# Performance work log

Hardware: AMD Instinct MI355X
Metric: run time of the kernel (lower is better)

Reference implementation:

```python
import jax, jax.numpy as jnp
import numpy as np

K = 8       # out_caps
H = 64      # nhidden
TAU = 1.0

def _l2norm(x, eps=1e-12):
    n = jnp.linalg.norm(x, axis=-1, keepdims=True)
    return x / jnp.maximum(n, eps)

def setup_inputs() -> dict:
    key = jax.random.key(0)
    k1, k2, k3, k4 = jax.random.split(key, 4)
    B, N, NB, D = 128, 50, 32, K * H
    return {
        "self_vectors": jax.random.normal(k1, (B, N, D), dtype=jnp.float32),
        "neighbor_vectors": jax.random.normal(k2, (B, N, NB, D), dtype=jnp.float32),
        "W1": jax.random.normal(k3, (D, D), dtype=jnp.float32) * 0.04,
        "b1": jax.random.normal(k4, (D,), dtype=jnp.float32) * 0.01,
        "max_iter": 3,
    }

def reference(self_vectors, neighbor_vectors, W1, b1, max_iter):
    B, N, _ = self_vectors.shape
    NB = neighbor_vectors.shape[2]
    # fc1 + ReLU projections (dropout p=0 -> identity)
    self_z = jax.nn.relu(self_vectors @ W1.T + b1)            # [B,N,K*H]
    neigh_z = jax.nn.relu(neighbor_vectors @ W1.T + b1)       # [B,N,NB,K*H]
    s = _l2norm(self_z.reshape(B, N, K, H))                   # [B,N,K,H]
    nz = _l2norm(neigh_z.reshape(B, N, NB, K, H))             # [B,N,NB,K,H]
    u = None
    for it in range(max_iter):
        if u is None:
            p = jnp.zeros((B, N, NB, K), dtype=s.dtype)
        else:
            p = jnp.einsum('bnmkh,bnkh->bnmk', nz, u)
        p = jax.nn.softmax(p / TAU, axis=-1)                   # softmax over K
        u = jnp.einsum('bnmkh,bnmk->bnkh', nz, p) + s          # sum over neighbors
        if it < max_iter - 1:
            u = _l2norm(u)
    return jax.nn.relu(u.reshape(B, N, K * H))
```

## Files before the change

### kernel.cpp

```cpp
#include <hip/hip_runtime.h>
#include <hip/hip_bf16.h>


#define D_DIM 512
#define BM 64
#define BK 32
#define KSTEPS 16

typedef __attribute__((ext_vector_type(8))) short short8;
typedef __attribute__((ext_vector_type(4))) short short4v;
typedef __attribute__((ext_vector_type(4))) float f32x4;

static __device__ __forceinline__ short f2bf(float f) {
    __bf16 b = (__bf16)f;
    return __builtin_bit_cast(short, b);
}
static __device__ __forceinline__ float bf2f(short s) {
    unsigned u = ((unsigned)(unsigned short)s) << 16;
    return __builtin_bit_cast(float, u);
}
static __device__ __forceinline__ void gload_lds16(const void* g, void* l) {
    __builtin_amdgcn_global_load_lds(
        (const __attribute__((address_space(1))) void*)g,
        (__attribute__((address_space(3))) void*)l, 16, 0, 0);
}

__global__ __launch_bounds__(256) void wconv(const float* __restrict__ W,
                                             short* __restrict__ Wb) {
    const int i = (blockIdx.x * 256 + threadIdx.x) * 8;
    const float4 v0 = *reinterpret_cast<const float4*>(W + i);
    const float4 v1 = *reinterpret_cast<const float4*>(W + i + 4);
    short8 o;
    o[0] = f2bf(v0.x); o[1] = f2bf(v0.y); o[2] = f2bf(v0.z); o[3] = f2bf(v0.w);
    o[4] = f2bf(v1.x); o[5] = f2bf(v1.y); o[6] = f2bf(v1.z); o[7] = f2bf(v1.w);
    *reinterpret_cast<short8*>(Wb + i) = o;
}

template <bool FUSED>
__global__ __launch_bounds__(256, 2) void gemm_route(
    const float* __restrict__ A,
    const short* __restrict__ Wb,
    const float* __restrict__ bias,
    short* __restrict__ Zs,
    const short* __restrict__ S,
    const int* __restrict__ miter_ptr,
    float* __restrict__ out)
{
    __shared__ __align__(16) char smem[81920];
    float* const lAf32 = (float*)smem;
    short* const lB = (short*)(smem + 16384);

    const int t = threadIdx.x;
    const int lane = t & 63;
    const int wid = t >> 6;
    const size_t row0 = (size_t)blockIdx.x * BM;
    const int wc = wid * 128;
    const int l15 = lane & 15;

    const int cb = wc + l15;
    float bcol[8];
    #pragma unroll
    for (int n = 0; n < 8; ++n) bcol[n] = bias[cb + n * 16];
    int miter = 0;
    if (FUSED) miter = *miter_ptr;

    auto stage = [&](int step, int buf) {
        const int k0 = step * BK;
        #pragma unroll
        for (int i = 0; i < 8; ++i) {
            const int c = wid * 8 + i;
            const int r = c * 16 + (lane >> 2);
            const int g = ((lane & 3) - (r >> 1)) & 3;
            gload_lds16(Wb + (size_t)r * D_DIM + k0 + g * 8,
                        lB + buf * 16384 + c * 512);
        }
        #pragma unroll
        for (int i = 0; i < 2; ++i) {
            const int c = wid * 2 + i;
            const int r = c * 8 + (lane >> 3);
            const int g = ((lane & 7) - (lane >> 3)) & 7;
            gload_lds16(A + (row0 + r) * D_DIM + k0 + g * 4,
                        lAf32 + buf * 2048 + c * 256);
        }
    };

    f32x4 acc[4][8] = {};
    auto compute = [&](int buf) {
        const int sq = lane >> 4;
        short8 af[4], bfr[8];
        #pragma unroll
        for (int m = 0; m < 4; ++m) {
            const int r = m * 16 + l15;
            const float* rowp = lAf32 + buf * 2048 + r * 32;
            const int P0 = (2 * sq + r) & 7;
            const int P1 = (2 * sq + 1 + r) & 7;
            const f32x4 a0 = *reinterpret_cast<const f32x4*>(rowp + P0 * 4);
            const f32x4 a1 = *reinterpret_cast<const f32x4*>(rowp + P1 * 4);
            short8 f;
            f[0] = f2bf(a0[0]); f[1] = f2bf(a0[1]);
            f[2] = f2bf(a0[2]); f[3] = f2bf(a0[3]);
            f[4] = f2bf(a1[0]); f[5] = f2bf(a1[1]);
            f[6] = f2bf(a1[2]); f[7] = f2bf(a1[3]);
            af[m] = f;
        }
        #pragma unroll
        for (int n = 0; n < 8; ++n) {
            const int r = wc + n * 16 + l15;
            bfr[n] = *reinterpret_cast<const short8*>(
                lB + buf * 16384 + r * 32 + ((sq + (r >> 1)) & 3) * 8);
        }
        #pragma unroll
        for (int m = 0; m < 4; ++m)
            #pragma unroll
            for (int n = 0; n < 8; ++n)
                acc[m][n] = __builtin_amdgcn_mfma_f32_16x16x32_bf16(
                    af[m], bfr[n], acc[m][n], 0, 0, 0);
    };

    stage(0, 0);
    stage(1, 1);
    asm volatile("s_waitcnt vmcnt(10)" ::: "memory");
    __builtin_amdgcn_s_barrier();
    #pragma unroll
    for (int tk = 0; tk < KSTEPS - 2; ++tk) {
        compute(tk & 1);
        asm volatile("s_waitcnt lgkmcnt(0)" ::: "memory");
        __builtin_amdgcn_s_barrier();
        stage(tk + 2, tk & 1);
        asm volatile("s_waitcnt vmcnt(10)" ::: "memory");
        __builtin_amdgcn_s_barrier();
    }
    compute(0);
    asm volatile("s_waitcnt lgkmcnt(0)" ::: "memory");
    __builtin_amdgcn_s_barrier();
    asm volatile("s_waitcnt vmcnt(0)" ::: "memory");
    __builtin_amdgcn_s_barrier();
    compute(1);
    asm volatile("s_waitcnt lgkmcnt(0)" ::: "memory");
    __builtin_amdgcn_s_barrier();

    short* const zbuf = (short*)(smem + 16384);
    #pragma unroll
    for (int m = 0; m < 4; ++m) {
        #pragma unroll
        for (int r = 0; r < 4; ++r) {
            float v[8];
            float ssa = 0.0f, ssb = 0.0f;
            #pragma unroll
            for (int n = 0; n < 4; ++n) {
                v[n] = fmaxf(acc[m][n][r] + bcol[n], 0.0f);
                ssa = fmaf(v[n], v[n], ssa);
            }
            #pragma unroll
            for (int n = 4; n < 8; ++n) {
                v[n] = fmaxf(acc[m][n][r] + bcol[n], 0.0f);
                ssb = fmaf(v[n], v[n], ssb);
            }
            ssa += __shfl_xor(ssa, 1); ssb += __shfl_xor(ssb, 1);
            ssa += __shfl_xor(ssa, 2); ssb += __shfl_xor(ssb, 2);
            ssa += __shfl_xor(ssa, 4); ssb += __shfl_xor(ssb, 4);
            ssa += __shfl_xor(ssa, 8); ssb += __shfl_xor(ssb, 8);
            const float inva = 1.0f / fmaxf(sqrtf(ssa), 1e-12f);
            const float invb = 1.0f / fmaxf(sqrtf(ssb), 1e-12f);
            const int orow = m * 16 + (lane >> 4) * 4 + r;
            if (FUSED) {
                #pragma unroll
                for (int n = 0; n < 4; ++n)
                    zbuf[orow * D_DIM + cb + n * 16] = f2bf(v[n] * inva);
                #pragma unroll
                for (int n = 4; n < 8; ++n)
                    zbuf[orow * D_DIM + cb + n * 16] = f2bf(v[n] * invb);
            } else {
                #pragma unroll
                for (int n = 0; n < 4; ++n)
                    Zs[(row0 + orow) * D_DIM + cb + n * 16] = f2bf(v[n] * inva);
                #pragma unroll
                for (int n = 4; n < 8; ++n)
                    Zs[(row0 + orow) * D_DIM + cb + n * 16] = f2bf(v[n] * invb);
            }
        }
    }

    if (!FUSED) return;
    __syncthreads();

    float* const scratch = (float*)smem;
    const int tt = t & 127;
    const int ssid = t >> 7;
    const size_t site = (size_t)blockIdx.x * 2 + ssid;
    float* const u_ = scratch + ssid * 512;
    float* const p_ = (float*)(smem + 4096) + ssid * 256;
    const short* const zr = zbuf + ssid * 32 * D_DIM;

    const int e = tt * 4;
    const int go = tt >> 4;
    const short4v sv = *reinterpret_cast<const short4v*>(S + site * D_DIM + e);
    const float s0 = bf2f(sv[0]), s1 = bf2f(sv[1]);
    const float s2 = bf2f(sv[2]), s3 = bf2f(sv[3]);

    float v0, v1, v2, v3;
    {
        float a0 = 0, a1 = 0, a2 = 0, a3 = 0;
        for (int m = 0; m < 32; ++m) {
            const short4v z = *reinterpret_cast<const short4v*>(zr + m * D_DIM + e);
            a0 += bf2f(z[0]); a1 += bf2f(z[1]); a2 += bf2f(z[2]); a3 += bf2f(z[3]);
        }
        v0 = fmaf(a0, 0.125f, s0); v1 = fmaf(a1, 0.125f, s1);
        v2 = fmaf(a2, 0.125f, s2); v3 = fmaf(a3, 0.125f, s3);
    }

    const int dm = tt >> 2;
    const int ka = (tt & 3) * 2;

    for (int it = 1; it < miter; ++it) {
        float ssum = v0 * v0 + v1 * v1 + v2 * v2 + v3 * v3;
        ssum += __shfl_xor(ssum, 1);
        ssum += __shfl_xor(ssum, 2);
        ssum += __shfl_xor(ssum, 4);
        ssum += __shfl_xor(ssum, 8);
        const float inv = 1.0f / fmaxf(sqrtf(ssum), 1e-12f);
        v0 *= inv; v1 *= inv; v2 *= inv; v3 *= inv;
        *reinterpret_cast<float4*>(u_ + e) = make_float4(v0, v1, v2, v3);
        __syncthreads();

        const short* const za = zr + dm * D_DIM + ka * 64;
        const float* const ua = u_ + ka * 64;
        float da = 0, db = 0;
        #pragma unroll
        for (int j = 0; j < 8; ++j) {
            const int jj = ((j + (tt & 7)) & 7) * 8;
            const short8 zva = *reinterpret_cast<const short8*>(za + jj);
            const short8 zvb = *reinterpret_cast<const short8*>(za + 64 + jj);
            const f32x4 uA0 = *reinterpret_cast<const f32x4*>(ua + jj);
            const f32x4 uA1 = *reinterpret_cast<const f32x4*>(ua + jj + 4);
            const f32x4 uB0 = *reinterpret_cast<const f32x4*>(ua + 64 + jj);
            const f32x4 uB1 = *reinterpret_cast<const f32x4*>(ua + 64 + jj + 4);
            #pragma unroll
            for (int qq = 0; qq < 4; ++qq) {
                da = fmaf(bf2f(zva[qq]), uA0[qq], da);
                da = fmaf(bf2f(zva[qq + 4]), uA1[qq], da);
                db = fmaf(bf2f(zvb[qq]), uB0[qq], db);
                db = fmaf(bf2f(zvb[qq + 4]), uB1[qq], db);
            }
        }
        float mx = fmaxf(da, db);
        mx = fmaxf(mx, __shfl_xor(mx, 1));
        mx = fmaxf(mx, __shfl_xor(mx, 2));
        const float ea = __expf(da - mx), eb = __expf(db - mx);
        float sm_ = ea + eb;
        sm_ += __shfl_xor(sm_, 1);
        sm_ += __shfl_xor(sm_, 2);
        const float rs = 1.0f / sm_;
        *reinterpret_cast<float2*>(p_ + dm * 8 + ka) = make_float2(ea * rs, eb * rs);
        __syncthreads();

        float a0 = 0, a1 = 0, a2 = 0, a3 = 0;
        for (int m = 0; m < 32; ++m) {
            const short4v z = *reinterpret_cast<const short4v*>(zr + m * D_DIM + e);
            const float pm = p_[m * 8 + go];
            a0 = fmaf(bf2f(z[0]), pm, a0); a1 = fmaf(bf2f(z[1]), pm, a1);
            a2 = fmaf(bf2f(z[2]), pm, a2); a3 = fmaf(bf2f(z[3]), pm, a3);
        }
        v0 = s0 + a0; v1 = s1 + a1; v2 = s2 + a2; v3 = s3 + a3;
    }

    *reinterpret_cast<float4*>(out + site * D_DIM + e) =
        make_float4(fmaxf(v0, 0.0f), fmaxf(v1, 0.0f),
                    fmaxf(v2, 0.0f), fmaxf(v3, 0.0f));
}

extern "C" void kernel_launch(void* const* d_in, const int* in_sizes, int n_in,
                              void* d_out, int out_size, void* d_ws, size_t ws_size,
                              hipStream_t stream) {
    const float* self_v  = (const float*)d_in[0];
    const float* neigh_v = (const float*)d_in[1];
    const float* W1      = (const float*)d_in[2];
    const float* b1      = (const float*)d_in[3];
    const int*   miter   = (const int*)d_in[4];
    float* out = (float*)d_out;

    const int sites = in_sizes[0] / D_DIM;
    const int nrows = in_sizes[1] / D_DIM;

    short* s  = (short*)d_ws;
    short* Wb = s + (size_t)sites * D_DIM;

    wconv<<<dim3(D_DIM * D_DIM / (256 * 8)), dim3(256), 0, stream>>>(W1, Wb);
    gemm_route<false><<<dim3(sites / BM), dim3(256), 0, stream>>>(
        self_v, Wb, b1, s, nullptr, nullptr, nullptr);
    gemm_route<true><<<dim3(nrows / BM), dim3(256), 0, stream>>>(
        neigh_v, Wb, b1, nullptr, s, miter, out);
}
```

Baseline: 251.5 us.

## Load weight fragments directly from global memory instead of staging through LDS

The bf16 weight tile is no longer copied into LDS with async global-to-LDS loads. Each wave now reads its B fragments straight from global memory into registers inside the compute step, and only the fp32 activations stay double-buffered in LDS. Wait counts are adjusted to the smaller number of staged loads, and the final barrier before the epilogue is dropped. This removes LDS traffic and capacity for B, but the global loads sit directly on the MFMA critical path with little latency hiding, and their strided access pattern may coalesce poorly.

```diff
diff --git a/kernel.cpp b/kernel.cpp
--- a/kernel.cpp
+++ b/kernel.cpp
@@ -48,7 +48,7 @@
 {
     __shared__ __align__(16) char smem[81920];
     float* const lAf32 = (float*)smem;
-    short* const lB = (short*)(smem + 16384);
+    short* const zbuf = (short*)(smem + 16384);
 
     const int t = threadIdx.x;
     const int lane = t & 63;
@@ -56,6 +56,7 @@
     const size_t row0 = (size_t)blockIdx.x * BM;
     const int wc = wid * 128;
     const int l15 = lane & 15;
+    const int q = lane >> 4;
 
     const int cb = wc + l15;
     float bcol[8];
@@ -64,16 +65,8 @@
     int miter = 0;
     if (FUSED) miter = *miter_ptr;
 
-    auto stage = [&](int step, int buf) {
+    auto stageA = [&](int step, int buf) {
         const int k0 = step * BK;
-        #pragma unroll
-        for (int i = 0; i < 8; ++i) {
-            const int c = wid * 8 + i;
-            const int r = c * 16 + (lane >> 2);
-            const int g = ((lane & 3) - (r >> 1)) & 3;
-            gload_lds16(Wb + (size_t)r * D_DIM + k0 + g * 8,
-                        lB + buf * 16384 + c * 512);
-        }
         #pragma unroll
         for (int i = 0; i < 2; ++i) {
             const int c = wid * 2 + i;
@@ -84,16 +77,22 @@
         }
     };
 
+    const short* const bBase = Wb + (size_t)(wc + l15) * D_DIM + q * 8;
+
     f32x4 acc[4][8] = {};
-    auto compute = [&](int buf) {
-        const int sq = lane >> 4;
-        short8 af[4], bfr[8];
+    auto compute = [&](int buf, int k0) {
+        short8 bfr[8];
+        #pragma unroll
+        for (int n = 0; n < 8; ++n)
+            bfr[n] = *reinterpret_cast<const short8*>(
+                bBase + (size_t)n * 16 * D_DIM + k0);
+        short8 af[4];
         #pragma unroll
         for (int m = 0; m < 4; ++m) {
             const int r = m * 16 + l15;
             const float* rowp = lAf32 + buf * 2048 + r * 32;
-            const int P0 = (2 * sq + r) & 7;
-            const int P1 = (2 * sq + 1 + r) & 7;
+            const int P0 = (2 * q + r) & 7;
+            const int P1 = (2 * q + 1 + r) & 7;
             const f32x4 a0 = *reinterpret_cast<const f32x4*>(rowp + P0 * 4);
             const f32x4 a1 = *reinterpret_cast<const f32x4*>(rowp + P1 * 4);
             short8 f;
@@ -104,12 +103,6 @@
             af[m] = f;
         }
         #pragma unroll
-        for (int n = 0; n < 8; ++n) {
-            const int r = wc + n * 16 + l15;
-            bfr[n] = *reinterpret_cast<const short8*>(
-                lB + buf * 16384 + r * 32 + ((sq + (r >> 1)) & 3) * 8);
-        }
-        #pragma unroll
         for (int m = 0; m < 4; ++m)
             #pragma unroll
             for (int n = 0; n < 8; ++n)
@@ -117,29 +110,27 @@
                     af[m], bfr[n], acc[m][n], 0, 0, 0);
     };
 
-    stage(0, 0);
-    stage(1, 1);
-    asm volatile("s_waitcnt vmcnt(10)" ::: "memory");
+    stageA(0, 0);
+    stageA(1, 1);
+    asm volatile("s_waitcnt vmcnt(2)" ::: "memory");
     __builtin_amdgcn_s_barrier();
     #pragma unroll
     for (int tk = 0; tk < KSTEPS - 2; ++tk) {
-        compute(tk & 1);
+        compute(tk & 1, tk * BK);
         asm volatile("s_waitcnt lgkmcnt(0)" ::: "memory");
         __builtin_amdgcn_s_barrier();
-        stage(tk + 2, tk & 1);
-        asm volatile("s_waitcnt vmcnt(10)" ::: "memory");
+        stageA(tk + 2, tk & 1);
+        __builtin_amdgcn_sched_barrier(0);
+        asm volatile("s_waitcnt vmcnt(2)" ::: "memory");
         __builtin_amdgcn_s_barrier();
     }
-    compute(0);
+    compute(0, 14 * BK);
     asm volatile("s_waitcnt lgkmcnt(0)" ::: "memory");
     __builtin_amdgcn_s_barrier();
     asm volatile("s_waitcnt vmcnt(0)" ::: "memory");
     __builtin_amdgcn_s_barrier();
-    compute(1);
-    asm volatile("s_waitcnt lgkmcnt(0)" ::: "memory");
-    __builtin_amdgcn_s_barrier();
-
-    short* const zbuf = (short*)(smem + 16384);
+    compute(1, 15 * BK);
+
     #pragma unroll
     for (int m = 0; m < 4; ++m) {
         #pragma unroll
@@ -162,7 +153,7 @@
             ssa += __shfl_xor(ssa, 8); ssb += __shfl_xor(ssb, 8);
             const float inva = 1.0f / fmaxf(sqrtf(ssa), 1e-12f);
             const float invb = 1.0f / fmaxf(sqrtf(ssb), 1e-12f);
-            const int orow = m * 16 + (lane >> 4) * 4 + r;
+            const int orow = m * 16 + q * 4 + r;
             if (FUSED) {
                 #pragma unroll
                 for (int n = 0; n < 4; ++n)
```

After: 341.0 us. +35.6%, slower.
